# Optimization experiments

Hardware: AMD Instinct MI355X
Metric: run time of the kernel (lower is better)

## Reference

```python
import jax, jax.numpy as jnp
import numpy as np

SEQ_LEN, BATCH, VOCAB, EMB, HID, LAYERS = 128, 128, 10000, 512, 512, 2

def setup_inputs() -> dict:
    key = jax.random.key(0)
    ks = jax.random.split(key, 8)
    k = float(np.sqrt(1.0 / HID))
    inputs = jax.random.randint(ks[0], (SEQ_LEN, BATCH), 0, VOCAB)
    hidden = jnp.zeros((LAYERS, BATCH, HID), dtype=jnp.float32)
    emb = jax.random.uniform(ks[1], (VOCAB, EMB), jnp.float32, -0.1, 0.1)
    W0 = jax.random.uniform(ks[2], (HID, EMB + HID), jnp.float32, -k, k)
    b0 = jax.random.uniform(ks[3], (HID,), jnp.float32, -k, k)
    W1 = jax.random.uniform(ks[4], (HID, 2 * HID), jnp.float32, -k, k)
    b1 = jax.random.uniform(ks[5], (HID,), jnp.float32, -k, k)
    Wout = jax.random.uniform(ks[6], (VOCAB, HID), jnp.float32, -0.1, 0.1)
    bout = jnp.zeros((VOCAB,), dtype=jnp.float32)
    return {"inputs": inputs, "hidden": hidden, "emb": emb, "W0": W0, "b0": b0,
            "W1": W1, "b1": b1, "Wout": Wout, "bout": bout}

def reference(inputs, hidden, emb, W0, b0, W1, b1, Wout, bout):
    # inputs: [S,B] int; hidden: [L,B,H]
    def step(h, tok):
        x = emb[tok]                                              # [B,E]
        h0 = jnp.tanh(jnp.concatenate([x, h[0]], axis=1) @ W0.T + b0)   # [B,H]
        h1 = jnp.tanh(jnp.concatenate([h0, h[1]], axis=1) @ W1.T + b1)  # [B,H]
        logits_t = h1 @ Wout.T + bout                             # [B,V]
        return jnp.stack([h0, h1]), logits_t
    hidden_final, logits = jax.lax.scan(step, hidden, inputs)
    return logits, hidden_final
```

## Files before the change

kernel.cpp:

```cpp
#include <hip/hip_runtime.h>
#include <hip/hip_fp16.h>

typedef _Float16 f16;
typedef _Float16 f16x4 __attribute__((ext_vector_type(4)));
typedef _Float16 f16x8 __attribute__((ext_vector_type(8)));
typedef float f32x4 __attribute__((ext_vector_type(4)));
typedef unsigned u32x4 __attribute__((ext_vector_type(4)));

#define S_LEN 128
#define B_SZ  128
#define VOC   10000
#define VPAD  10240
#define HIDN  512
#define NBLK  64

__device__ __forceinline__ void gload_lds16(const void* g, void* l) {
  __builtin_amdgcn_global_load_lds(
      (const __attribute__((address_space(1))) void*)g,
      (__attribute__((address_space(3))) void*)l, 16, 0, 0);
}

__device__ __forceinline__ f16x8 ld16_dev(const f16* p) {
  u32x4 r;
  asm volatile("global_load_dwordx4 %0, %1, off sc1" : "=v"(r) : "v"(p));
  return __builtin_bit_cast(f16x8, r);
}
__device__ __forceinline__ void cstore2(f16* p, float v) {
  f16 h = (f16)v;
  unsigned short u = __builtin_bit_cast(unsigned short, h);
  __hip_atomic_store((unsigned short*)p, u, __ATOMIC_RELAXED, __HIP_MEMORY_SCOPE_AGENT);
}

__device__ __forceinline__ float fast_tanh(float x) {
  float cx = fminf(8.f, fmaxf(-8.f, x));
  float e = __expf(2.f * cx);
  float d = e + 1.f, r;
  asm("v_rcp_f32 %0, %1" : "=v"(r) : "v"(d));
  return (e - 1.f) * r;
}

__global__ void convert_pad(const float* __restrict__ src, f16* __restrict__ dst,
                            int rows, int src_stride, int total) {
  int idx = blockIdx.x * 256 + threadIdx.x;
  if (idx >= total) return;
  int r = idx >> 9, c = idx & 511;
  float v = (r < rows) ? src[(size_t)r * src_stride + c] : 0.f;
  dst[idx] = (f16)v;
}

template <typename CT>
__global__ __launch_bounds__(256) void gemm_k512(
    const f16* __restrict__ A, const f16* __restrict__ B,
    CT* __restrict__ C, const float* __restrict__ bias,
    int M, int N, int ldc)
{
  __shared__ f16 Asw[128 * 32];
  __shared__ f16 Bsw[128 * 32];
  const int tid  = threadIdx.x;
  const int lane = tid & 63, w = tid >> 6;
  const int wrow = w >> 1, wcol = w & 1;
  int nwg  = gridDim.x * gridDim.y;
  int orig = blockIdx.y * gridDim.x + blockIdx.x;
  int cpx  = nwg >> 3;
  int swz  = (orig & 7) * cpx + (orig >> 3);
  const int m0 = (swz / gridDim.x) * 128, n0 = (swz % gridDim.x) * 128;
  const int rsel = lane & 15, ksl = lane >> 4;

  f32x4 acc[4][4] = {};

  for (int kt = 0; kt < 16; ++kt) {
    __syncthreads();
#pragma unroll
    for (int i = 0; i < 2; ++i) {
      int c   = (i * 4 + w) * 64 + lane;
      int row = c >> 2, sp = c & 3;
      int sl  = sp ^ ((row >> 1) & 3);
      gload_lds16(A + (size_t)(m0 + row) * 512 + kt * 32 + sl * 8,
                  &Asw[(i * 4 + w) * 512]);
      gload_lds16(B + (size_t)(n0 + row) * 512 + kt * 32 + sl * 8,
                  &Bsw[(i * 4 + w) * 512]);
    }
    __syncthreads();
    f16x8 af[4], bf[4];
#pragma unroll
    for (int i = 0; i < 4; ++i) {
      int ar = wrow * 64 + i * 16 + rsel;
      af[i] = *(const f16x8*)&Asw[ar * 32 + ((ksl ^ ((ar >> 1) & 3)) * 8)];
      int br = wcol * 64 + i * 16 + rsel;
      bf[i] = *(const f16x8*)&Bsw[br * 32 + ((ksl ^ ((br >> 1) & 3)) * 8)];
    }
#pragma unroll
    for (int i = 0; i < 4; ++i)
#pragma unroll
      for (int j = 0; j < 4; ++j)
        acc[i][j] = __builtin_amdgcn_mfma_f32_16x16x32_f16(af[i], bf[j], acc[i][j], 0, 0, 0);
  }

#pragma unroll
  for (int tc = 0; tc < 4; ++tc) {
    int col = n0 + wcol * 64 + tc * 16 + rsel;
    if (col >= N) continue;
    float bv = bias ? bias[col] : 0.f;
#pragma unroll
    for (int i = 0; i < 4; ++i) {
      int rowb = m0 + wrow * 64 + i * 16 + ksl * 4;
#pragma unroll
      for (int j = 0; j < 4; ++j) {
        int row = rowb + j;
        if (row < M) C[(size_t)row * ldc + col] = (CT)(acc[i][tc][j] + bv);
      }
    }
  }
}

__global__ __launch_bounds__(256, 1) void rnn_recur(
    const int* __restrict__ tok,
    const float* __restrict__ W0,
    const float* __restrict__ W1,
    const float* __restrict__ b1,
    const f16* __restrict__ P0h,
    f16* __restrict__ h0ring,
    const f16* __restrict__ h1init,
    f16* __restrict__ H1,
    float* __restrict__ outHid,
    unsigned* __restrict__ cnt)
{
  __shared__ f16 wlds[3][16 * 512];
  const int tid = threadIdx.x;
  const int lane = tid & 63, w = tid >> 6;
  const int cgI = blockIdx.x & 31, bg = blockIdx.x >> 5;
  const int col0 = cgI * 16;
  const int rowstart = bg * 64 + w * 16;
  const int rsel = lane & 15, ksl = lane >> 4;

  for (int it = tid; it < 3 * 16 * 64; it += 256) {
    int s = it >> 10;
    int rem = it & 1023;
    int c = rem >> 6, ks = rem & 63;
    int n = col0 + c;
    const float* srcp;
    if (s == 0)      srcp = W0 + (size_t)n * 1024 + 512 + ks * 8;
    else if (s == 1) srcp = W1 + (size_t)n * 1024 + ks * 8;
    else             srcp = W1 + (size_t)n * 1024 + 512 + ks * 8;
    f16x8 v;
#pragma unroll
    for (int j = 0; j < 8; ++j) v[j] = (f16)srcp[j];
    *(f16x8*)&wlds[s][c * 512 + ((ks ^ (c & 7)) * 8)] = v;
  }
  float b1v = b1[col0 + rsel];
  __syncthreads();

  const int rbase = rowstart + ksl * 4;
  const size_t hrow = (size_t)(rowstart + rsel) * HIDN;

  f16x8 hf[16];
  f32x4 part1;

  for (int p = 0; p <= S_LEN + 1; ++p) {
    const bool doH0 = (p <= S_LEN - 1);
    const bool doH1 = (p >= 2);

    if (doH1) {
      f32x4 t = {b1v, b1v, b1v, b1v};
#pragma unroll
      for (int kt = 0; kt < 16; ++kt) {
        int ks = kt * 4 + ksl;
        f16x8 b = *(const f16x8*)&wlds[1][rsel * 512 + ((ks ^ (rsel & 7)) * 8)];
        t = __builtin_amdgcn_mfma_f32_16x16x32_f16(hf[kt], b, t, 0, 0, 0);
      }
      part1 = t;
    }
    f32x4 p0acc;
    if (doH0) {
#pragma unroll
      for (int j = 0; j < 4; ++j) {
        int t_ = tok[p * B_SZ + rbase + j];
        p0acc[j] = (float)P0h[(size_t)t_ * HIDN + col0 + rsel];
      }
    }

    if (p >= 1) {
      if (tid == 0) {
        unsigned tgt = (unsigned)(NBLK * p);
        while (__hip_atomic_load(cnt, __ATOMIC_RELAXED, __HIP_MEMORY_SCOPE_AGENT) < tgt) {}
      }
      __syncthreads();
    }

    if (p <= S_LEN) {
      const f16* src = h0ring + (size_t)((p - 1) & 3) * B_SZ * HIDN;
#pragma unroll
      for (int kt = 0; kt < 16; ++kt)
        hf[kt] = ld16_dev(src + hrow + kt * 32 + ksl * 8);
    }
    f16x8 h1f[16];
    if (doH1) {
      const f16* h1src = (p == 2) ? h1init : H1 + (size_t)(p - 3) * B_SZ * HIDN;
#pragma unroll
      for (int kt = 0; kt < 16; ++kt)
        h1f[kt] = ld16_dev(h1src + hrow + kt * 32 + ksl * 8);
    }
    asm volatile("s_waitcnt vmcnt(0)" ::: "memory");
    __builtin_amdgcn_sched_barrier(0);

    if (doH0) {
      f32x4 acc0 = p0acc;
#pragma unroll
      for (int kt = 0; kt < 16; ++kt) {
        int ks = kt * 4 + ksl;
        f16x8 b = *(const f16x8*)&wlds[0][rsel * 512 + ((ks ^ (rsel & 7)) * 8)];
        acc0 = __builtin_amdgcn_mfma_f32_16x16x32_f16(hf[kt], b, acc0, 0, 0, 0);
      }
      f16* dst = h0ring + (size_t)(p & 3) * B_SZ * HIDN;
#pragma unroll
      for (int j = 0; j < 4; ++j) {
        float v = fast_tanh(acc0[j]);
        int r = rbase + j;
        cstore2(&dst[(size_t)r * HIDN + col0 + rsel], v);
        if (p == S_LEN - 1) outHid[(size_t)r * HIDN + col0 + rsel] = v;
      }
    }
    if (doH1) {
      f32x4 acc1 = part1;
#pragma unroll
      for (int kt = 0; kt < 16; ++kt) {
        int ks = kt * 4 + ksl;
        f16x8 b = *(const f16x8*)&wlds[2][rsel * 512 + ((ks ^ (rsel & 7)) * 8)];
        acc1 = __builtin_amdgcn_mfma_f32_16x16x32_f16(h1f[kt], b, acc1, 0, 0, 0);
      }
      f16* h1dst = H1 + (size_t)(p - 2) * B_SZ * HIDN;
#pragma unroll
      for (int j = 0; j < 4; ++j) {
        float v = fast_tanh(acc1[j]);
        int r = rbase + j;
        cstore2(&h1dst[(size_t)r * HIDN + col0 + rsel], v);
        if (p == S_LEN + 1) outHid[(size_t)(B_SZ * HIDN) + (size_t)r * HIDN + col0 + rsel] = v;
      }
    }

    if (p <= S_LEN) {
      asm volatile("s_waitcnt vmcnt(0)" ::: "memory");
      __syncthreads();
      if (tid == 0)
        __hip_atomic_fetch_add(cnt, 1u, __ATOMIC_RELAXED, __HIP_MEMORY_SCOPE_AGENT);
    }
  }
}

extern "C" void kernel_launch(void* const* d_in, const int* in_sizes, int n_in,
                              void* d_out, int out_size, void* d_ws, size_t ws_size,
                              hipStream_t stream) {
  (void)in_sizes; (void)n_in; (void)out_size; (void)ws_size;
  const int*   tok    = (const int*)d_in[0];
  const float* hidden = (const float*)d_in[1];
  const float* emb    = (const float*)d_in[2];
  const float* W0     = (const float*)d_in[3];
  const float* b0     = (const float*)d_in[4];
  const float* W1     = (const float*)d_in[5];
  const float* b1     = (const float*)d_in[6];
  const float* Wout   = (const float*)d_in[7];
  const float* bout   = (const float*)d_in[8];

  char* ws = (char*)d_ws;
  size_t off = 0;
  f16* embf16  = (f16*)(ws + off); off += (size_t)VPAD * 512 * 2;
  f16* woutf16 = (f16*)(ws + off); off += (size_t)VPAD * 512 * 2;
  f16* w0xf16  = (f16*)(ws + off); off += (size_t)512 * 512 * 2;
  f16* P0h     = (f16*)(ws + off); off += (size_t)VOC * 512 * 2;
  f16* H1      = (f16*)(ws + off); off += (size_t)S_LEN * B_SZ * 512 * 2;
  f16* h0ring  = (f16*)(ws + off); off += (size_t)4 * B_SZ * 512 * 2;
  f16* h1init  = (f16*)(ws + off); off += (size_t)B_SZ * 512 * 2;
  unsigned* cnt = (unsigned*)(ws + off); off += 64;

  float* outHid = (float*)d_out + (size_t)S_LEN * B_SZ * VOC;

  hipMemsetAsync(cnt, 0, 4, stream);

  int tot = VPAD * 512;
  convert_pad<<<(tot + 255) / 256, 256, 0, stream>>>(emb,  embf16,  VOC, 512, tot);
  convert_pad<<<(tot + 255) / 256, 256, 0, stream>>>(Wout, woutf16, VOC, 512, tot);
  tot = 512 * 512;
  convert_pad<<<(tot + 255) / 256, 256, 0, stream>>>(W0, w0xf16, 512, 1024, tot);
  tot = B_SZ * 512;
  convert_pad<<<(tot + 255) / 256, 256, 0, stream>>>(hidden, h0ring + (size_t)3 * B_SZ * 512, B_SZ, 512, tot);
  convert_pad<<<(tot + 255) / 256, 256, 0, stream>>>(hidden + (size_t)B_SZ * 512, h1init, B_SZ, 512, tot);

  gemm_k512<f16><<<dim3(4, VPAD / 128), 256, 0, stream>>>(
      embf16, w0xf16, P0h, b0, VOC, 512, 512);

  {
    void* args[] = {(void*)&tok, (void*)&W0, (void*)&W1, (void*)&b1, (void*)&P0h,
                    (void*)&h0ring, (void*)&h1init, (void*)&H1, (void*)&outHid, (void*)&cnt};
    hipLaunchCooperativeKernel((const void*)rnn_recur, dim3(NBLK), dim3(256), args, 0, stream);
  }

  gemm_k512<float><<<dim3(79, 128), 256, 0, stream>>>(
      H1, woutf16, (float*)d_out, bout, S_LEN * B_SZ, VOC, VOC);
}
```

Measured before the change: 1.300 ms.

## Replace global atomic counter barrier with per-wave flag array polled by every wave

The single atomic counter plus __syncthreads grid barrier is replaced by per-wave step flags. Each wave writes its own flag with a plain sc1 store, and every wave polls all 256 flags with one dwordx4 load per lane, so there is no block-level sync and no atomic contention. The single vmcnt(0) wait is also split into partial waits, so the h0 MFMA chain can start before the h1 loads land. This removes atomic serialization and intra-block barrier latency from the per-timestep critical path. In exchange, every wave now polls global memory, and correctness depends on the ordering of the vmcnt counts.

```diff
diff --git a/kernel.cpp b/kernel.cpp
--- a/kernel.cpp
+++ b/kernel.cpp
@@ -13,6 +13,10 @@
 #define VPAD  10240
 #define HIDN  512
 #define NBLK  64
+#define NFLAG (NBLK * 4)
+
+#define VMCNT(n) do { asm volatile("s_waitcnt vmcnt(" #n ")" ::: "memory"); \
+                      __builtin_amdgcn_sched_barrier(0); } while (0)
 
 __device__ __forceinline__ void gload_lds16(const void* g, void* l) {
   __builtin_amdgcn_global_load_lds(
@@ -29,6 +33,9 @@
   f16 h = (f16)v;
   unsigned short u = __builtin_bit_cast(unsigned short, h);
   __hip_atomic_store((unsigned short*)p, u, __ATOMIC_RELAXED, __HIP_MEMORY_SCOPE_AGENT);
+}
+__device__ __forceinline__ void stflag_dev(unsigned* p, unsigned v) {
+  asm volatile("global_store_dword %0, %1, off sc1" :: "v"(p), "v"(v) : "memory");
 }
 
 __device__ __forceinline__ float fast_tanh(float x) {
@@ -123,7 +130,7 @@
     const f16* __restrict__ h1init,
     f16* __restrict__ H1,
     float* __restrict__ outHid,
-    unsigned* __restrict__ cnt)
+    unsigned* __restrict__ flags)
 {
   __shared__ f16 wlds[3][16 * 512];
   const int tid = threadIdx.x;
@@ -132,6 +139,7 @@
   const int col0 = cgI * 16;
   const int rowstart = bg * 64 + w * 16;
   const int rsel = lane & 15, ksl = lane >> 4;
+  const int fidx = blockIdx.x * 4 + w;
 
   for (int it = tid; it < 3 * 16 * 64; it += 256) {
     int s = it >> 10;
@@ -152,6 +160,7 @@
 
   const int rbase = rowstart + ksl * 4;
   const size_t hrow = (size_t)(rowstart + rsel) * HIDN;
+  const unsigned* fptr = flags + 4 * lane;
 
   f16x8 hf[16];
   f32x4 part1;
@@ -170,21 +179,25 @@
       }
       part1 = t;
     }
-    f32x4 p0acc;
+    float pa0, pa1, pa2, pa3;
     if (doH0) {
-#pragma unroll
-      for (int j = 0; j < 4; ++j) {
-        int t_ = tok[p * B_SZ + rbase + j];
-        p0acc[j] = (float)P0h[(size_t)t_ * HIDN + col0 + rsel];
-      }
+      const int tbase = p * B_SZ + rbase;
+      pa0 = (float)P0h[(size_t)tok[tbase + 0] * HIDN + col0 + rsel];
+      pa1 = (float)P0h[(size_t)tok[tbase + 1] * HIDN + col0 + rsel];
+      pa2 = (float)P0h[(size_t)tok[tbase + 2] * HIDN + col0 + rsel];
+      pa3 = (float)P0h[(size_t)tok[tbase + 3] * HIDN + col0 + rsel];
+      asm volatile("" : "+v"(pa0), "+v"(pa1), "+v"(pa2), "+v"(pa3));
     }
 
     if (p >= 1) {
-      if (tid == 0) {
-        unsigned tgt = (unsigned)(NBLK * p);
-        while (__hip_atomic_load(cnt, __ATOMIC_RELAXED, __HIP_MEMORY_SCOPE_AGENT) < tgt) {}
-      }
-      __syncthreads();
+      const unsigned tgt = (unsigned)p;
+      for (;;) {
+        u32x4 f;
+        asm volatile("global_load_dwordx4 %0, %1, off sc1\n\ts_waitcnt vmcnt(0)"
+                     : "=v"(f) : "v"(fptr) : "memory");
+        int ok = (f[0] >= tgt) & (f[1] >= tgt) & (f[2] >= tgt) & (f[3] >= tgt);
+        if (__all(ok)) break;
+      }
     }
 
     if (p <= S_LEN) {
@@ -200,11 +213,10 @@
       for (int kt = 0; kt < 16; ++kt)
         h1f[kt] = ld16_dev(h1src + hrow + kt * 32 + ksl * 8);
     }
-    asm volatile("s_waitcnt vmcnt(0)" ::: "memory");
-    __builtin_amdgcn_sched_barrier(0);
 
     if (doH0) {
-      f32x4 acc0 = p0acc;
+      if (doH1) { VMCNT(16); } else { VMCNT(0); }
+      f32x4 acc0 = {pa0, pa1, pa2, pa3};
 #pragma unroll
       for (int kt = 0; kt < 16; ++kt) {
         int ks = kt * 4 + ksl;
@@ -221,6 +233,7 @@
       }
     }
     if (doH1) {
+      if (doH0) { VMCNT(8); } else { VMCNT(0); }
       f32x4 acc1 = part1;
 #pragma unroll
       for (int kt = 0; kt < 16; ++kt) {
@@ -239,10 +252,8 @@
     }
 
     if (p <= S_LEN) {
-      asm volatile("s_waitcnt vmcnt(0)" ::: "memory");
-      __syncthreads();
-      if (tid == 0)
-        __hip_atomic_fetch_add(cnt, 1u, __ATOMIC_RELAXED, __HIP_MEMORY_SCOPE_AGENT);
+      VMCNT(0);
+      if (lane == 0) stflag_dev((unsigned*)flags + fidx, (unsigned)(p + 1));
     }
   }
 }
@@ -270,11 +281,11 @@
   f16* H1      = (f16*)(ws + off); off += (size_t)S_LEN * B_SZ * 512 * 2;
   f16* h0ring  = (f16*)(ws + off); off += (size_t)4 * B_SZ * 512 * 2;
   f16* h1init  = (f16*)(ws + off); off += (size_t)B_SZ * 512 * 2;
-  unsigned* cnt = (unsigned*)(ws + off); off += 64;
+  unsigned* flags = (unsigned*)(ws + off); off += NFLAG * 4;
 
   float* outHid = (float*)d_out + (size_t)S_LEN * B_SZ * VOC;
 
-  hipMemsetAsync(cnt, 0, 4, stream);
+  hipMemsetAsync(flags, 0, NFLAG * 4, stream);
 
   int tot = VPAD * 512;
   convert_pad<<<(tot + 255) / 256, 256, 0, stream>>>(emb,  embf16,  VOC, 512, tot);
@@ -290,7 +301,7 @@
 
   {
     void* args[] = {(void*)&tok, (void*)&W0, (void*)&W1, (void*)&b1, (void*)&P0h,
-                    (void*)&h0ring, (void*)&h1init, (void*)&H1, (void*)&outHid, (void*)&cnt};
+                    (void*)&h0ring, (void*)&h1init, (void*)&H1, (void*)&outHid, (void*)&flags};
     hipLaunchCooperativeKernel((const void*)rnn_recur, dim3(NBLK), dim3(256), args, 0, stream);
   }
 
```

Result: faster. 1.205 ms (-7.3%).
